# Optimization experiments

Measured on AMD Instinct MI355X. Metric: run time of the kernel, lower is better.

Reference implementation:

```python
import jax, jax.numpy as jnp
import numpy as np

K = 20
EPS = 1e-5
NEG_SLOPE = 0.2


def _bn(x, gamma, beta, axes):
    # batch-norm in training mode (batch statistics), per-channel on last axis
    mean = jnp.mean(x, axis=axes, keepdims=True)
    var = jnp.var(x, axis=axes, keepdims=True)
    return gamma * (x - mean) * jax.lax.rsqrt(var + EPS) + beta


def _lrelu(x):
    return jnp.where(x >= 0, x, NEG_SLOPE * x)


def setup_inputs() -> dict:
    key = jax.random.key(0)
    ks = jax.random.split(key, 8)
    B, C, N = 8, 6, 4096

    def w(k_, shape):
        fan_in = shape[-1]
        return jax.random.normal(k_, shape, jnp.float32) / np.sqrt(fan_in)

    return {
        "x": jax.random.normal(ks[0], (B, C, N), jnp.float32),
        "conv1_w": w(ks[1], (64, 12)),
        "bn1_g": jnp.ones((64,), jnp.float32), "bn1_b": jnp.zeros((64,), jnp.float32),
        "conv2_w": w(ks[2], (128, 64)),
        "bn2_g": jnp.ones((128,), jnp.float32), "bn2_b": jnp.zeros((128,), jnp.float32),
        "conv3_w": w(ks[3], (1024, 128)),
        "bn3_g": jnp.ones((1024,), jnp.float32), "bn3_b": jnp.zeros((1024,), jnp.float32),
        "fc1_w": w(ks[4], (512, 1024)),
        "bn4_g": jnp.ones((512,), jnp.float32), "bn4_b": jnp.zeros((512,), jnp.float32),
        "fc2_w": w(ks[5], (256, 512)),
        "bn5_g": jnp.ones((256,), jnp.float32), "bn5_b": jnp.zeros((256,), jnp.float32),
        "fc3_w": w(ks[6], (9, 256)), "fc3_b": jnp.zeros((9,), jnp.float32),
        "fc4_w": w(ks[7], (3, 256)), "fc4_b": jnp.zeros((3,), jnp.float32),
    }


def _get_graph_feature(x, k):
    # x: [B, C, N] -> [B, N, k, 2C]
    B, C, N = x.shape
    xt = jnp.transpose(x, (0, 2, 1))                      # [B, N, C]
    xx = jnp.sum(xt * xt, axis=-1)                        # [B, N]
    inner = jnp.einsum('bnc,bmc->bnm', xt, xt)            # [B, N, N]
    pd = 2.0 * inner - xx[:, :, None] - xx[:, None, :]    # -||xi-xj||^2
    _, idx = jax.lax.top_k(pd, k)                         # [B, N, k]
    nbr = xt[jnp.arange(B)[:, None, None], idx]           # [B, N, k, C]
    center = jnp.broadcast_to(xt[:, :, None, :], nbr.shape)
    return jnp.concatenate([nbr - center, center], axis=-1)  # [B, N, k, 2C]


def reference(x, conv1_w, bn1_g, bn1_b, conv2_w, bn2_g, bn2_b,
              conv3_w, bn3_g, bn3_b, fc1_w, bn4_g, bn4_b,
              fc2_w, bn5_g, bn5_b, fc3_w, fc3_b, fc4_w, fc4_b):
    B = x.shape[0]
    feat = _get_graph_feature(x, K)                            # [B, N, k, 12]
    h = _lrelu(_bn(jnp.einsum('bnkc,oc->bnko', feat, conv1_w), bn1_g, bn1_b, (0, 1, 2)))
    h = _lrelu(_bn(jnp.einsum('bnkc,oc->bnko', h, conv2_w), bn2_g, bn2_b, (0, 1, 2)))
    h = jnp.max(h, axis=2)                                     # [B, N, 128] max over k
    h = _lrelu(_bn(jnp.einsum('bnc,oc->bno', h, conv3_w), bn3_g, bn3_b, (0, 1)))
    g = jnp.max(h, axis=1)                                     # [B, 1024] max over points
    g = _lrelu(_bn(g @ fc1_w.T, bn4_g, bn4_b, (0,)))           # [B, 512]
    g = _lrelu(_bn(g @ fc2_w.T, bn5_g, bn5_b, (0,)))           # [B, 256]
    bias = (g @ fc4_w.T + fc4_b)[:, None, :]                   # [B, 1, 3]
    matrix = jnp.eye(3, dtype=x.dtype) + (g @ fc3_w.T + fc3_b).reshape(B, 3, 3)
    xyz = jnp.transpose(x[:, :3, :], (0, 2, 1))                # [B, N, 3]
    out = jnp.einsum('bnc,bcd->bnd', xyz, matrix) + bias       # [B, N, 3]
    return jnp.transpose(out, (0, 2, 1))                       # [B, 3, N]
```

## Files before the change

### kernel.cpp

```cpp
#include <hip/hip_runtime.h>
#include <math.h>
#include <stddef.h>


static constexpr float EPS_ = 1e-5f;

__global__ __launch_bounds__(256) void k_prep(const float* __restrict__ x,
                                              float* __restrict__ xtp,
                                              const float* __restrict__ w2,
                                              float* __restrict__ w2t)
{
    int i = blockIdx.x*256 + threadIdx.x;
    int b = i >> 12, n = i & 4095;
    const float* xb = x + (size_t)b*6*4096 + n;
    float v0 = xb[0], v1 = xb[4096], v2 = xb[2*4096];
    float v3 = xb[3*4096], v4 = xb[4*4096], v5 = xb[5*4096];
    float xx = v0*v0 + v1*v1 + v2*v2 + v3*v3 + v4*v4 + v5*v5;
    float4* o = (float4*)(xtp + (size_t)i*8);
    o[0] = make_float4(v0, v1, v2, v3);
    o[1] = make_float4(v4, v5, xx, 0.f);
    if (blockIdx.x < 2){
        int e = blockIdx.x*256 + threadIdx.x;
        for (int q = e; q < 64*128; q += 512){
            int c = q >> 7, oo = q & 127;
            w2t[q] = w2[oo*64 + c];
        }
    }
}

__device__ __forceinline__ float pd_calc(const float4 a0, const float4 a1,
                                         const float4 q0, const float4 q1)
{
    float dot = a0.x*q0.x;
    dot = fmaf(a0.y, q0.y, dot);
    dot = fmaf(a0.z, q0.z, dot);
    dot = fmaf(a0.w, q0.w, dot);
    dot = fmaf(a1.x, q1.x, dot);
    dot = fmaf(a1.y, q1.y, dot);
    return fmaf(2.f, dot, -a1.z - q1.z);
}

__device__ __forceinline__ unsigned fkey_(float f){
    unsigned u = __float_as_uint(f);
    return (u & 0x80000000u) ? ~u : (u | 0x80000000u);
}
__device__ __forceinline__ float finv_(unsigned k){
    return (k & 0x80000000u) ? __uint_as_float(k & 0x7fffffffu)
                             : __uint_as_float(~k);
}

#define TK_CAP 384
__global__ __launch_bounds__(256) void k_topk(const float* __restrict__ xtp,
                                              int* __restrict__ idxout)
{
    __shared__ float maxs[4][256];
    __shared__ float candv[4][TK_CAP];
    __shared__ int   candi[4][TK_CAP];
    __shared__ float Ts[4];
    __shared__ unsigned ccnt[4], ocnt[4], nwork;
    __shared__ unsigned short work[1024];

    const int t = threadIdx.x;
    const int rowbase = blockIdx.x << 2;
    const int b = rowbase >> 12;
    const float* xb = xtp + ((size_t)b << 15);

    float4 c0[4], c1[4];
    #pragma unroll
    for (int c = 0; c < 4; c++){
        const float4* p = (const float4*)(xtp + (size_t)(rowbase + c)*8);
        c0[c] = p[0]; c1[c] = p[1];
    }
    if (t < 4){ ccnt[t] = 0u; ocnt[t] = 0u; }
    if (t == 0) nwork = 0u;

    float mx[4] = {-INFINITY, -INFINITY, -INFINITY, -INFINITY};
    {
        const float4* qp = (const float4*)(xb + (size_t)t*8);
        for (int i = 0; i < 16; i++){
            float4 q0 = qp[0], q1 = qp[1];
            #pragma unroll
            for (int c = 0; c < 4; c++)
                mx[c] = fmaxf(mx[c], pd_calc(c0[c], c1[c], q0, q1));
            qp += 512;
        }
    }
    #pragma unroll
    for (int c = 0; c < 4; c++) maxs[c][t] = mx[c];
    __syncthreads();

    const int w = t >> 6, lane = t & 63;
    {
        unsigned k0 = fkey_(maxs[w][lane]);
        unsigned k1 = fkey_(maxs[w][64  + lane]);
        unsigned k2 = fkey_(maxs[w][128 + lane]);
        unsigned k3 = fkey_(maxs[w][192 + lane]);
        unsigned lo = 0u;
        for (int bit = 31; bit >= 0; bit--){
            unsigned cand = lo | (1u << bit);
            int cnt = __popcll(__ballot(k0 >= cand))
                    + __popcll(__ballot(k1 >= cand))
                    + __popcll(__ballot(k2 >= cand))
                    + __popcll(__ballot(k3 >= cand));
            if (cnt >= 20) lo = cand;
        }
        if (lane == 0) Ts[w] = finv_(lo);
    }
    __syncthreads();

    #pragma unroll
    for (int c = 0; c < 4; c++){
        if (mx[c] >= Ts[c]){
            unsigned pos = atomicAdd(&nwork, 1u);
            work[pos] = (unsigned short)((c << 8) | t);
        }
    }
    __syncthreads();

    {
        int total = (int)nwork << 4;
        for (int e = t; e < total; e += 256){
            int ct = work[e >> 4];
            int c = ct >> 8, src = ct & 255;
            int m = ((e & 15) << 8) | src;
            const float4* p = (const float4*)(xb + (size_t)m*8);
            float4 q0 = p[0], q1 = p[1];
            float pd = pd_calc(c0[c], c1[c], q0, q1);
            if (pd >= Ts[c]){
                unsigned pos = atomicAdd(&ccnt[c], 1u);
                if (pos < TK_CAP){ candv[c][pos] = pd; candi[c][pos] = m; }
            }
        }
    }
    __syncthreads();

    {
        int n = (int)min(ccnt[w], (unsigned)TK_CAP);
        unsigned key[6]; int id[6];
        #pragma unroll
        for (int j = 0; j < 6; j++){
            int p = (j << 6) | lane;
            bool ok = p < n;
            key[j] = ok ? fkey_(candv[w][p]) : 0u;
            id[j]  = ok ? candi[w][p] : 0x7fffffff;
        }
        unsigned C = 0u;
        for (int bit = 31; bit >= 0; bit--){
            unsigned cand = C | (1u << bit);
            int cnt = 0;
            #pragma unroll
            for (int j = 0; j < 6; j++)
                cnt += __popcll(__ballot(key[j] >= cand));
            if (cnt >= 20) C = cand;
        }
        int m = 0, e = 0;
        #pragma unroll
        for (int j = 0; j < 6; j++){
            m += __popcll(__ballot(key[j] > C));
            e += __popcll(__ballot(key[j] == C));
        }
        int* outp = idxout + (size_t)(rowbase + w)*20;
        #pragma unroll
        for (int j = 0; j < 6; j++){
            if (key[j] > C){
                unsigned pos = atomicAdd(&ocnt[w], 1u);
                outp[pos] = id[j];
            }
        }
        int need = 20 - m;
        if (e <= need){
            #pragma unroll
            for (int j = 0; j < 6; j++){
                if (key[j] == C){
                    unsigned pos = atomicAdd(&ocnt[w], 1u);
                    outp[pos] = id[j];
                }
            }
        } else {
            for (int r = 0; r < need; r++){
                int loc = 0x7fffffff;
                #pragma unroll
                for (int j = 0; j < 6; j++)
                    if (key[j] == C && id[j] < loc) loc = id[j];
                int g = loc;
                #pragma unroll
                for (int s = 1; s < 64; s <<= 1) g = min(g, __shfl_xor(g, s));
                #pragma unroll
                for (int j = 0; j < 6; j++){
                    if (key[j] == C && id[j] == g){
                        key[j] = 0u;
                        unsigned pos = atomicAdd(&ocnt[w], 1u);
                        outp[pos] = g;
                    }
                }
            }
        }
    }
}

__global__ __launch_bounds__(256) void k_bn1stats(const float* __restrict__ xtp,
                                                  const int* __restrict__ idxb,
                                                  const float* __restrict__ w1,
                                                  float* __restrict__ bn1sum,
                                                  float* __restrict__ bn1sq)
{
    __shared__ float fT[320*12];
    __shared__ float red[2][4][64];
    const int t = threadIdx.x;
    const int rowbase = blockIdx.x << 4;
    const int b = rowbase >> 12;

    for (int s = t; s < 320; s += 256){
        int r = s / 20, k = s % 20;
        int grow = rowbase + r;
        int m = idxb[(size_t)grow*20 + k];
        const float4* pn = (const float4*)(xtp + (size_t)((b << 12) | m)*8);
        const float4* pc = (const float4*)(xtp + (size_t)grow*8);
        float4 n0 = pn[0], n1 = pn[1], c0 = pc[0], c1 = pc[1];
        float* f = fT + s*12;
        ((float4*)f)[0] = make_float4(n0.x-c0.x, n0.y-c0.y, n0.z-c0.z, n0.w-c0.w);
        ((float4*)f)[1] = make_float4(n1.x-c1.x, n1.y-c1.y, c0.x, c0.y);
        ((float4*)f)[2] = make_float4(c0.z, c0.w, c1.x, c1.y);
    }
    __syncthreads();
    const int o = t & 63, grp = t >> 6;
    float w[12];
    #pragma unroll
    for (int c = 0; c < 12; c++) w[c] = w1[o*12 + c];
    float sm = 0.f, sq = 0.f;
    for (int s = grp*80; s < grp*80 + 80; s++){
        const float* f = fT + s*12;
        float4 f0 = *(const float4*)(f);
        float4 fa = *(const float4*)(f + 4);
        float4 fb = *(const float4*)(f + 8);
        float h = w[0]*f0.x + w[1]*f0.y + w[2]*f0.z + w[3]*f0.w
                + w[4]*fa.x + w[5]*fa.y + w[6]*fa.z + w[7]*fa.w
                + w[8]*fb.x + w[9]*fb.y + w[10]*fb.z + w[11]*fb.w;
        sm += h; sq = fmaf(h, h, sq);
    }
    red[0][grp][o] = sm; red[1][grp][o] = sq;
    __syncthreads();
    if (t < 64){
        float a = red[0][0][t] + red[0][1][t] + red[0][2][t] + red[0][3][t];
        float c2 = red[1][0][t] + red[1][1][t] + red[1][2][t] + red[1][3][t];
        atomicAdd(bn1sum + t, a);
        atomicAdd(bn1sq + t, c2);
    }
}

__global__ void k_bnfin(const float* __restrict__ sum, const float* __restrict__ sq,
                        const float* __restrict__ gamma, const float* __restrict__ beta,
                        float* __restrict__ st, int C, float invN)
{
    int o = threadIdx.x;
    if (o < C){
        float mean = sum[o]*invN;
        float var  = sq[o]*invN - mean*mean;
        float s = gamma[o]/sqrtf(var + EPS_);
        st[o] = s;
        st[C + o] = beta[o] - mean*s;
    }
}

__global__ __launch_bounds__(256, 3) void k_conv12(
    const float* __restrict__ xtp, const int* __restrict__ idxb,
    const float* __restrict__ w1, const float* __restrict__ w2t,
    const float* __restrict__ bn1st,
    float* __restrict__ h2max, float* __restrict__ bn2sum, float* __restrict__ bn2sq)
{
    __shared__ float f1s[5120];
    __shared__ float w2u[8192];
    const int t = threadIdx.x;
    const int rowbase = blockIdx.x << 2;
    const int b = rowbase >> 12;

    const int j = t & 63;
    float wr[12];
    #pragma unroll
    for (int c = 0; c < 12; c++) wr[c] = w1[j*12 + c];

    float* fT = w2u;
    if (t < 80){
        int r = t / 20;
        int grow = rowbase + r;
        int m = idxb[(size_t)grow*20 + (t - r*20)];
        const float4* pn = (const float4*)(xtp + (size_t)((b << 12) | m)*8);
        const float4* pc = (const float4*)(xtp + (size_t)grow*8);
        float4 n0 = pn[0], n1 = pn[1], c0 = pc[0], c1 = pc[1];
        float* f = fT + t*12;
        ((float4*)f)[0] = make_float4(n0.x-c0.x, n0.y-c0.y, n0.z-c0.z, n0.w-c0.w);
        ((float4*)f)[1] = make_float4(n1.x-c1.x, n1.y-c1.y, c0.x, c0.y);
        ((float4*)f)[2] = make_float4(c0.z, c0.w, c1.x, c1.y);
    }
    __syncthreads();
    {
        const float s1 = bn1st[j], t1 = bn1st[64 + j];
        for (int vid = t; vid < 5120; vid += 256){
            const float* f = fT + (vid >> 6)*12;
            float4 f0 = *(const float4*)(f);
            float4 fa = *(const float4*)(f + 4);
            float4 fb = *(const float4*)(f + 8);
            float acc = wr[0]*f0.x + wr[1]*f0.y + wr[2]*f0.z + wr[3]*f0.w
                      + wr[4]*fa.x + wr[5]*fa.y + wr[6]*fa.z + wr[7]*fa.w
                      + wr[8]*fb.x + wr[9]*fb.y + wr[10]*fb.z + wr[11]*fb.w;
            float v = fmaf(s1, acc, t1);
            f1s[vid] = fmaxf(v, 0.2f*v);
        }
    }
    __syncthreads();
    {
        float4 tmp[8];
        #pragma unroll
        for (int i = 0; i < 8; i++) tmp[i] = ((const float4*)w2t)[t + (i << 8)];
        #pragma unroll
        for (int i = 0; i < 8; i++) ((float4*)w2u)[t + (i << 8)] = tmp[i];
    }
    __syncthreads();

    const int oq = t & 31, kslot = t >> 5;
    const int o0 = oq << 2;
    float mx[4][4], sm[4][4], sq[4][4];
    #pragma unroll
    for (int r = 0; r < 4; r++)
        #pragma unroll
        for (int i = 0; i < 4; i++){ mx[r][i] = -INFINITY; sm[r][i] = 0.f; sq[r][i] = 0.f; }
    for (int k = kslot; k < 20; k += 8){
        float h[4][4];
        #pragma unroll
        for (int r = 0; r < 4; r++){ h[r][0]=0.f; h[r][1]=0.f; h[r][2]=0.f; h[r][3]=0.f; }
        for (int jl = 0; jl < 64; jl += 4){
            float wv[4][4];
            #pragma unroll
            for (int jj = 0; jj < 4; jj++)
                *(float4*)wv[jj] = *(const float4*)&w2u[(jl + jj)*128 + o0];
            #pragma unroll
            for (int r = 0; r < 4; r++){
                float fv[4];
                *(float4*)fv = *(const float4*)&f1s[((r*20 + k) << 6) + jl];
                #pragma unroll
                for (int jj = 0; jj < 4; jj++)
                    #pragma unroll
                    for (int oi = 0; oi < 4; oi++)
                        h[r][oi] = fmaf(fv[jj], wv[jj][oi], h[r][oi]);
            }
        }
        #pragma unroll
        for (int r = 0; r < 4; r++)
            #pragma unroll
            for (int oi = 0; oi < 4; oi++){
                mx[r][oi] = fmaxf(mx[r][oi], h[r][oi]);
                sm[r][oi] += h[r][oi];
                sq[r][oi] = fmaf(h[r][oi], h[r][oi], sq[r][oi]);
            }
    }
    __syncthreads();
    #pragma unroll
    for (int r = 0; r < 4; r++){
        int base = ((kslot << 2) + r)*128 + o0;
        *(float4*)&f1s[base] = make_float4(mx[r][0], mx[r][1], mx[r][2], mx[r][3]);
        *(float4*)&w2u[base] = make_float4(sm[r][0], sm[r][1], sm[r][2], sm[r][3]);
        *(float4*)&w2u[4096 + base] = make_float4(sq[r][0], sq[r][1], sq[r][2], sq[r][3]);
    }
    __syncthreads();
    for (int it = t; it < 512; it += 256){
        int r = it >> 7, o = it & 127;
        float m = f1s[r*128 + o];
        #pragma unroll
        for (int ks = 1; ks < 8; ks++) m = fmaxf(m, f1s[((ks << 2) + r)*128 + o]);
        h2max[(size_t)(rowbase + r)*128 + o] = m;
    }
    if (t < 128){
        float s = 0.f, q = 0.f;
        #pragma unroll
        for (int i = 0; i < 32; i++){ s += w2u[i*128 + t]; q += w2u[4096 + i*128 + t]; }
        atomicAdd(bn2sum + t, s);
        atomicAdd(bn2sq + t, q);
    }
}

__global__ __launch_bounds__(256) void k_wt3(const float* __restrict__ w3,
                                             float* __restrict__ w3t)
{
    int i = blockIdx.x*256 + threadIdx.x;
    int j = i >> 10, o = i & 1023;
    w3t[i] = w3[(size_t)o*128 + j];
}

__global__ __launch_bounds__(256, 3) void k_conv3(const float* __restrict__ h2max,
    const float* __restrict__ bn2st, const float* __restrict__ w3t,
    float* __restrict__ bn3sum, float* __restrict__ bn3sq, unsigned int* __restrict__ gkey)
{
    __shared__ float f2[32*132];
    __shared__ float w3s[8192];
    const int t = threadIdx.x;
    const int bid = blockIdx.x;
    const int idx = bid >> 3;
    const int rt = (bid & 7)*128 + (idx >> 4);
    const int ot = idx & 15;
    const int rowbase = rt << 5;
    const int obase = ot << 6;
    const int b = rowbase >> 12;

    for (int e = t; e < 32*128; e += 256){
        int r = e >> 7, c = e & 127;
        float v = h2max[(size_t)(rowbase + r)*128 + c];
        float u = fmaf(bn2st[c], v, bn2st[128 + c]);
        f2[r*132 + c] = fmaxf(u, 0.2f*u);
    }
    {
        float4 tmp[8];
        #pragma unroll
        for (int i = 0; i < 8; i++){
            int q = t + (i << 8);
            tmp[i] = *(const float4*)&w3t[(size_t)(q >> 4)*1024 + obase + ((q & 15) << 2)];
        }
        #pragma unroll
        for (int i = 0; i < 8; i++) ((float4*)w3s)[t + (i << 8)] = tmp[i];
    }
    __syncthreads();

    const int oq = t & 15, rg = t >> 4;
    const int o0 = oq << 2, r0 = rg << 1;
    float h0[4] = {0.f,0.f,0.f,0.f}, h1[4] = {0.f,0.f,0.f,0.f};
    for (int jl = 0; jl < 128; jl += 4){
        float wv[4][4];
        #pragma unroll
        for (int jj = 0; jj < 4; jj++)
            *(float4*)wv[jj] = *(const float4*)&w3s[(jl + jj)*64 + o0];
        float fa[4], fb[4];
        *(float4*)fa = *(const float4*)&f2[r0*132 + jl];
        *(float4*)fb = *(const float4*)&f2[(r0 + 1)*132 + jl];
        #pragma unroll
        for (int jj = 0; jj < 4; jj++)
            #pragma unroll
            for (int oi = 0; oi < 4; oi++){
                h0[oi] = fmaf(fa[jj], wv[jj][oi], h0[oi]);
                h1[oi] = fmaf(fb[jj], wv[jj][oi], h1[oi]);
            }
    }
    __syncthreads();
    float* scr = f2;
    *(float4*)&scr[(rg << 6) + o0] =
        make_float4(h0[0]+h1[0], h0[1]+h1[1], h0[2]+h1[2], h0[3]+h1[3]);
    *(float4*)&scr[1024 + (rg << 6) + o0] =
        make_float4(h0[0]*h0[0]+h1[0]*h1[0], h0[1]*h0[1]+h1[1]*h1[1],
                    h0[2]*h0[2]+h1[2]*h1[2], h0[3]*h0[3]+h1[3]*h1[3]);
    *(float4*)&scr[2048 + (rg << 6) + o0] =
        make_float4(fmaxf(h0[0],h1[0]), fmaxf(h0[1],h1[1]),
                    fmaxf(h0[2],h1[2]), fmaxf(h0[3],h1[3]));
    __syncthreads();
    if (t < 192){
        int stat = t >> 6, o = t & 63;
        if (stat == 0){
            float s = 0.f;
            #pragma unroll
            for (int g2 = 0; g2 < 16; g2++) s += scr[(g2 << 6) + o];
            atomicAdd(bn3sum + obase + o, s);
        } else if (stat == 1){
            float s = 0.f;
            #pragma unroll
            for (int g2 = 0; g2 < 16; g2++) s += scr[1024 + (g2 << 6) + o];
            atomicAdd(bn3sq + obase + o, s);
        } else {
            float m = scr[2048 + o];
            #pragma unroll
            for (int g2 = 1; g2 < 16; g2++) m = fmaxf(m, scr[2048 + (g2 << 6) + o]);
            unsigned u = __float_as_uint(m);
            unsigned key = (u & 0x80000000u) ? ~u : (u | 0x80000000u);
            atomicMax(gkey + (b << 10) + obase + o, key);
        }
    }
}

__global__ void k_bn3g(const float* __restrict__ sum, const float* __restrict__ sq,
                       const unsigned int* __restrict__ gkey,
                       const float* __restrict__ gamma, const float* __restrict__ beta,
                       float* __restrict__ g)
{
    int o = blockIdx.x*256 + threadIdx.x;
    if (o < 1024){
        float mean = sum[o]*(1.f/32768.f);
        float var  = sq[o]*(1.f/32768.f) - mean*mean;
        float s = gamma[o]/sqrtf(var + EPS_);
        float tt = beta[o] - mean*s;
        for (int b = 0; b < 8; b++){
            unsigned k = gkey[(b << 10) + o];
            unsigned u = (k & 0x80000000u) ? (k & 0x7fffffffu) : ~k;
            float v = __uint_as_float(u);
            float xv = fmaf(s, v, tt);
            g[(b << 10) + o] = fmaxf(xv, 0.2f*xv);
        }
    }
}

__global__ __launch_bounds__(256) void k_fc(const float* __restrict__ in,
                                            const float* __restrict__ w,
                                            float* __restrict__ out, int Kdim, int Odim)
{
    int wid = (blockIdx.x*256 + threadIdx.x) >> 6;
    int lane = threadIdx.x & 63;
    int nout = 8*Odim;
    if (wid >= nout) return;
    int b = wid / Odim, o = wid - b*Odim;
    const float* gi = in + (size_t)b*Kdim;
    const float* wr = w + (size_t)o*Kdim;
    float acc = 0.f;
    for (int c = lane; c < Kdim; c += 64) acc = fmaf(gi[c], wr[c], acc);
    #pragma unroll
    for (int s = 32; s > 0; s >>= 1) acc += __shfl_xor(acc, s);
    if (lane == 0) out[(size_t)b*Odim + o] = acc;
}

__global__ void k_bnb(const float* __restrict__ h, const float* __restrict__ gamma,
                      const float* __restrict__ beta, float* __restrict__ g, int C)
{
    int o = blockIdx.x*256 + threadIdx.x;
    if (o < C){
        float s = 0.f, q = 0.f;
        for (int b = 0; b < 8; b++){ float v = h[(size_t)b*C + o]; s += v; q = fmaf(v, v, q); }
        float mean = s*0.125f;
        float var  = q*0.125f - mean*mean;
        float sc = gamma[o]/sqrtf(var + EPS_);
        float tt = beta[o] - mean*sc;
        for (int b = 0; b < 8; b++){
            float xv = fmaf(sc, h[(size_t)b*C + o], tt);
            g[(size_t)b*C + o] = fmaxf(xv, 0.2f*xv);
        }
    }
}

__global__ void k_head(const float* __restrict__ g5,
                       const float* __restrict__ fc3w, const float* __restrict__ fc3b,
                       const float* __restrict__ fc4w, const float* __restrict__ fc4b,
                       float* __restrict__ mat, float* __restrict__ bias3)
{
    int t = threadIdx.x;
    if (t < 96){
        int b = t / 12, j = t % 12;
        const float* gi = g5 + b*256;
        if (j < 9){
            const float* w = fc3w + j*256;
            float a = fc3b[j];
            for (int c = 0; c < 256; c++) a = fmaf(gi[c], w[c], a);
            if (j == 0 || j == 4 || j == 8) a += 1.f;
            mat[b*9 + j] = a;
        } else {
            int d = j - 9;
            const float* w = fc4w + d*256;
            float a = fc4b[d];
            for (int c = 0; c < 256; c++) a = fmaf(gi[c], w[c], a);
            bias3[b*3 + d] = a;
        }
    }
}

__global__ __launch_bounds__(256) void k_out(const float* __restrict__ x,
                                             const float* __restrict__ mat,
                                             const float* __restrict__ bias3,
                                             float* __restrict__ out)
{
    int i = blockIdx.x*256 + threadIdx.x;
    int n = i & 4095, bd = i >> 12;
    int b = bd / 3, d = bd - b*3;
    const float* xb = x + (size_t)b*6*4096 + n;
    const float* M = mat + b*9;
    out[i] = xb[0]*M[d] + xb[4096]*M[3 + d] + xb[2*4096]*M[6 + d] + bias3[b*3 + d];
}

extern "C" void kernel_launch(void* const* d_in, const int* in_sizes, int n_in,
                              void* d_out, int out_size, void* d_ws, size_t ws_size,
                              hipStream_t stream)
{
    const float* x     = (const float*)d_in[0];
    const float* w1    = (const float*)d_in[1];
    const float* bn1g  = (const float*)d_in[2];
    const float* bn1b  = (const float*)d_in[3];
    const float* w2    = (const float*)d_in[4];
    const float* bn2g  = (const float*)d_in[5];
    const float* bn2b  = (const float*)d_in[6];
    const float* w3    = (const float*)d_in[7];
    const float* bn3gm = (const float*)d_in[8];
    const float* bn3bt = (const float*)d_in[9];
    const float* fc1w  = (const float*)d_in[10];
    const float* bn4g  = (const float*)d_in[11];
    const float* bn4b  = (const float*)d_in[12];
    const float* fc2w  = (const float*)d_in[13];
    const float* bn5g  = (const float*)d_in[14];
    const float* bn5b  = (const float*)d_in[15];
    const float* fc3w  = (const float*)d_in[16];
    const float* fc3b  = (const float*)d_in[17];
    const float* fc4w  = (const float*)d_in[18];
    const float* fc4b  = (const float*)d_in[19];
    float* out = (float*)d_out;

    char* ws = (char*)d_ws;
    float* xtp   = (float*)(ws);
    float* w3t_g = (float*)(ws);
    int*   idxb  = (int*)  (ws + 1048576);
    float* h2max = (float*)(ws + 3670016);
    float* zs    = (float*)(ws + 20447232);
    float* bn1sum = zs;            float* bn1sq = zs + 64;
    float* bn2sum = zs + 128;      float* bn2sq = zs + 256;
    float* bn3sum = zs + 384;      float* bn3sq = zs + 1408;
    unsigned int* gkey = (unsigned int*)(zs + 2432);
    float* tail  = (float*)(ws + 20489728);
    float* bn1st = tail;
    float* bn2st = tail + 128;
    float* g     = tail + 384;
    float* h4    = tail + 8576;
    float* g4    = tail + 12672;
    float* h5    = tail + 16768;
    float* g5    = tail + 18816;
    float* mat   = tail + 20864;
    float* bias3 = tail + 20936;
    float* w2t_g = (float*)(ws + 20573568);

    hipMemsetAsync(zs, 0, 42496, stream);

    k_prep    <<<128,   256, 0, stream>>>(x, xtp, w2, w2t_g);
    k_topk    <<<8192,  256, 0, stream>>>(xtp, idxb);
    k_bn1stats<<<2048,  256, 0, stream>>>(xtp, idxb, w1, bn1sum, bn1sq);
    k_bnfin   <<<1,     128, 0, stream>>>(bn1sum, bn1sq, bn1g, bn1b, bn1st, 64, 1.f/655360.f);
    k_conv12  <<<8192,  256, 0, stream>>>(xtp, idxb, w1, w2t_g, bn1st, h2max, bn2sum, bn2sq);
    k_wt3     <<<512,   256, 0, stream>>>(w3, w3t_g);
    k_bnfin   <<<1,     128, 0, stream>>>(bn2sum, bn2sq, bn2g, bn2b, bn2st, 128, 1.f/655360.f);
    k_conv3   <<<16384, 256, 0, stream>>>(h2max, bn2st, w3t_g, bn3sum, bn3sq, gkey);
    k_bn3g    <<<4,     256, 0, stream>>>(bn3sum, bn3sq, gkey, bn3gm, bn3bt, g);
    k_fc      <<<1024,  256, 0, stream>>>(g, fc1w, h4, 1024, 512);
    k_bnb     <<<2,     256, 0, stream>>>(h4, bn4g, bn4b, g4, 512);
    k_fc      <<<512,   256, 0, stream>>>(g4, fc2w, h5, 512, 256);
    k_bnb     <<<1,     256, 0, stream>>>(h5, bn5g, bn5b, g5, 256);
    k_head    <<<1,     128, 0, stream>>>(g5, fc3w, fc3b, fc4w, fc4b, mat, bias3);
    k_out     <<<384,   256, 0, stream>>>(x, mat, bias3, out);
}
```

Before: 776.2 us.

## Retile conv2 GEMM to 5x8 register blocks with swizzled shared memory

Changes the conv2 inner product in k_conv12 so each thread computes 5 neighbor rows by 8 output channels, up from 4 by 4. The k loop that previously gave some threads 3 iterations and others 2 is gone. w2 is stored transposed and padded (stride 516), and f1 gets an XOR swizzle to cut LDS bank conflicts. Max, sum and sum-of-squares reductions are reorganised to match the new thread mapping. This raises register pressure (40 accumulators) under launch bounds of 3 blocks per CU.

```diff
diff --git a/kernel.cpp b/kernel.cpp
--- a/kernel.cpp
+++ b/kernel.cpp
@@ -268,16 +268,16 @@
     const float* __restrict__ bn1st,
     float* __restrict__ h2max, float* __restrict__ bn2sum, float* __restrict__ bn2sq)
 {
-    __shared__ float f1s[5120];
-    __shared__ float w2u[8192];
+    __shared__ float f1s[80*64];
+    __shared__ float w2u[16*516];
     const int t = threadIdx.x;
     const int rowbase = blockIdx.x << 2;
     const int b = rowbase >> 12;
 
-    const int j = t & 63;
+    const int jch = t & 63;
     float wr[12];
     #pragma unroll
-    for (int c = 0; c < 12; c++) wr[c] = w1[j*12 + c];
+    for (int c = 0; c < 12; c++) wr[c] = w1[jch*12 + c];
 
     float* fT = w2u;
     if (t < 80){
@@ -294,9 +294,10 @@
     }
     __syncthreads();
     {
-        const float s1 = bn1st[j], t1 = bn1st[64 + j];
+        const float s1 = bn1st[jch], t1 = bn1st[64 + jch];
         for (int vid = t; vid < 5120; vid += 256){
-            const float* f = fT + (vid >> 6)*12;
+            int vec = vid >> 6;
+            const float* f = fT + vec*12;
             float4 f0 = *(const float4*)(f);
             float4 fa = *(const float4*)(f + 4);
             float4 fb = *(const float4*)(f + 8);
@@ -304,7 +305,7 @@
                       + wr[4]*fa.x + wr[5]*fa.y + wr[6]*fa.z + wr[7]*fa.w
                       + wr[8]*fb.x + wr[9]*fb.y + wr[10]*fb.z + wr[11]*fb.w;
             float v = fmaf(s1, acc, t1);
-            f1s[vid] = fmaxf(v, 0.2f*v);
+            f1s[(vec << 6) + (jch ^ ((vec & 7) << 2))] = fmaxf(v, 0.2f*v);
         }
     }
     __syncthreads();
@@ -313,68 +314,90 @@
         #pragma unroll
         for (int i = 0; i < 8; i++) tmp[i] = ((const float4*)w2t)[t + (i << 8)];
         #pragma unroll
-        for (int i = 0; i < 8; i++) ((float4*)w2u)[t + (i << 8)] = tmp[i];
-    }
-    __syncthreads();
-
-    const int oq = t & 31, kslot = t >> 5;
-    const int o0 = oq << 2;
-    float mx[4][4], sm[4][4], sq[4][4];
-    #pragma unroll
-    for (int r = 0; r < 4; r++)
-        #pragma unroll
-        for (int i = 0; i < 4; i++){ mx[r][i] = -INFINITY; sm[r][i] = 0.f; sq[r][i] = 0.f; }
-    for (int k = kslot; k < 20; k += 8){
-        float h[4][4];
-        #pragma unroll
-        for (int r = 0; r < 4; r++){ h[r][0]=0.f; h[r][1]=0.f; h[r][2]=0.f; h[r][3]=0.f; }
-        for (int jl = 0; jl < 64; jl += 4){
-            float wv[4][4];
+        for (int i = 0; i < 8; i++){
+            int q = t + (i << 8);
+            int jr = q >> 5, o4 = q & 31;
+            *(float4*)&w2u[(o4 >> 1)*516 + (jr << 3) + ((o4 & 1) << 2)] = tmp[i];
+        }
+    }
+    __syncthreads();
+
+    const int vg = t & 15, og = t >> 4;
+    const float* fp = f1s + vg*5*64;
+    const float* wp = w2u + og*516;
+    int xw[5];
+    #pragma unroll
+    for (int i = 0; i < 5; i++) xw[i] = ((vg*5 + i) & 7) << 2;
+
+    float h[5][8];
+    #pragma unroll
+    for (int i = 0; i < 5; i++)
+        #pragma unroll
+        for (int oi = 0; oi < 8; oi++) h[i][oi] = 0.f;
+
+    #pragma unroll
+    for (int jl = 0; jl < 64; jl += 4){
+        float wv[4][8];
+        #pragma unroll
+        for (int jj = 0; jj < 4; jj++){
+            *(float4*)&wv[jj][0] = *(const float4*)&wp[((jl + jj) << 3)];
+            *(float4*)&wv[jj][4] = *(const float4*)&wp[((jl + jj) << 3) + 4];
+        }
+        #pragma unroll
+        for (int i = 0; i < 5; i++){
+            float fv[4];
+            *(float4*)fv = *(const float4*)&fp[(i << 6) + (jl ^ xw[i])];
             #pragma unroll
             for (int jj = 0; jj < 4; jj++)
-                *(float4*)wv[jj] = *(const float4*)&w2u[(jl + jj)*128 + o0];
-            #pragma unroll
-            for (int r = 0; r < 4; r++){
-                float fv[4];
-                *(float4*)fv = *(const float4*)&f1s[((r*20 + k) << 6) + jl];
                 #pragma unroll
-                for (int jj = 0; jj < 4; jj++)
-                    #pragma unroll
-                    for (int oi = 0; oi < 4; oi++)
-                        h[r][oi] = fmaf(fv[jj], wv[jj][oi], h[r][oi]);
-            }
-        }
-        #pragma unroll
-        for (int r = 0; r < 4; r++)
-            #pragma unroll
-            for (int oi = 0; oi < 4; oi++){
-                mx[r][oi] = fmaxf(mx[r][oi], h[r][oi]);
-                sm[r][oi] += h[r][oi];
-                sq[r][oi] = fmaf(h[r][oi], h[r][oi], sq[r][oi]);
-            }
-    }
-    __syncthreads();
-    #pragma unroll
-    for (int r = 0; r < 4; r++){
-        int base = ((kslot << 2) + r)*128 + o0;
-        *(float4*)&f1s[base] = make_float4(mx[r][0], mx[r][1], mx[r][2], mx[r][3]);
-        *(float4*)&w2u[base] = make_float4(sm[r][0], sm[r][1], sm[r][2], sm[r][3]);
-        *(float4*)&w2u[4096 + base] = make_float4(sq[r][0], sq[r][1], sq[r][2], sq[r][3]);
+                for (int oi = 0; oi < 8; oi++)
+                    h[i][oi] = fmaf(fv[jj], wv[jj][oi], h[i][oi]);
+        }
+    }
+
+    float mxl[8], sml[8], sql[8];
+    #pragma unroll
+    for (int oi = 0; oi < 8; oi++){
+        float v = h[0][oi];
+        mxl[oi] = v; sml[oi] = v; sql[oi] = v*v;
+    }
+    #pragma unroll
+    for (int i = 1; i < 5; i++)
+        #pragma unroll
+        for (int oi = 0; oi < 8; oi++){
+            float v = h[i][oi];
+            mxl[oi] = fmaxf(mxl[oi], v);
+            sml[oi] += v;
+            sql[oi] = fmaf(v, v, sql[oi]);
+        }
+    __syncthreads();
+    {
+        const int r = vg >> 2, q = vg & 3;
+        int base = (((q << 2) | r) << 7) + (og << 3);
+        *(float4*)&w2u[base]        = *(float4*)&mxl[0];
+        *(float4*)&w2u[base + 4]    = *(float4*)&mxl[4];
+        *(float4*)&w2u[2048 + base]     = *(float4*)&sml[0];
+        *(float4*)&w2u[2048 + base + 4] = *(float4*)&sml[4];
+        *(float4*)&w2u[4096 + base]     = *(float4*)&sql[0];
+        *(float4*)&w2u[4096 + base + 4] = *(float4*)&sql[4];
     }
     __syncthreads();
     for (int it = t; it < 512; it += 256){
         int r = it >> 7, o = it & 127;
-        float m = f1s[r*128 + o];
-        #pragma unroll
-        for (int ks = 1; ks < 8; ks++) m = fmaxf(m, f1s[((ks << 2) + r)*128 + o]);
+        float m = w2u[(r << 7) + o];
+        #pragma unroll
+        for (int q = 1; q < 4; q++) m = fmaxf(m, w2u[(((q << 2) | r) << 7) + o]);
         h2max[(size_t)(rowbase + r)*128 + o] = m;
     }
     if (t < 128){
-        float s = 0.f, q = 0.f;
-        #pragma unroll
-        for (int i = 0; i < 32; i++){ s += w2u[i*128 + t]; q += w2u[4096 + i*128 + t]; }
+        float s = 0.f, qq = 0.f;
+        #pragma unroll
+        for (int u = 0; u < 16; u++){
+            s  += w2u[2048 + (u << 7) + t];
+            qq += w2u[4096 + (u << 7) + t];
+        }
         atomicAdd(bn2sum + t, s);
-        atomicAdd(bn2sq + t, q);
+        atomicAdd(bn2sq + t, qq);
     }
 }
 
```

After: 774.6 us. Within noise of the previous version (-0.2%).
